# Kernel tuning notes

Hardware: AMD Instinct MI355X
Metric: run time of the kernel (lower is better)

## Reference

```python
import jax, jax.numpy as jnp
import numpy as np

D_MODEL = 1024
N_HEAD = 16
HEAD_SIZE = D_MODEL // N_HEAD
BLOCK_SIZE = 1024
NORM_EPS = 1e-6
B, T = 4, 1024


def setup_inputs() -> dict:
    key = jax.random.key(0)
    ks = jax.random.split(key, 16)
    s = 0.02
    d, h = D_MODEL, 4 * D_MODEL
    return {
        "x":  jax.random.normal(ks[0], (B, T, d), jnp.float32),
        "Wq": jax.random.normal(ks[1], (d, d), jnp.float32) * s,
        "bq": jax.random.normal(ks[2], (d,), jnp.float32) * s,
        "Wk": jax.random.normal(ks[3], (d, d), jnp.float32) * s,
        "bk": jax.random.normal(ks[4], (d,), jnp.float32) * s,
        "Wv": jax.random.normal(ks[5], (d, d), jnp.float32) * s,
        "bv": jax.random.normal(ks[6], (d,), jnp.float32) * s,
        "Wp": jax.random.normal(ks[7], (d, d), jnp.float32) * s,
        "bp": jax.random.normal(ks[8], (d,), jnp.float32) * s,
        "gamma": jnp.ones((d,), jnp.float32),
        "W1": jax.random.normal(ks[9], (d, h), jnp.float32) * s,
        "b1": jax.random.normal(ks[10], (h,), jnp.float32) * s,
        "W2": jax.random.normal(ks[11], (h, d), jnp.float32) * s,
        "b2": jax.random.normal(ks[12], (d,), jnp.float32) * s,
    }


def _rmsnorm(x, gamma):
    ms = jnp.mean(jnp.square(x), axis=-1, keepdims=True)
    return x * jax.lax.rsqrt(ms + NORM_EPS) * gamma


def _attn(x, Wq, bq, Wk, bk, Wv, bv, Wp, bp, causal):
    b, t, c = x.shape
    q = (x @ Wq + bq).reshape(b, t, N_HEAD, HEAD_SIZE)
    k = (x @ Wk + bk).reshape(b, t, N_HEAD, HEAD_SIZE)
    v = (x @ Wv + bv).reshape(b, t, N_HEAD, HEAD_SIZE)
    # NOTE: source divides by head_size**(-0.5) -> multiply by sqrt(head_size)
    scores = jnp.einsum("bqhd,bkhd->bhqk", q, k) * (HEAD_SIZE ** 0.5)
    if causal:
        tril = jnp.tril(jnp.ones((t, t), bool))
        scores = jnp.where(tril, scores, -jnp.inf)
    att = jax.nn.softmax(scores, axis=-1)
    out = jnp.einsum("bhqk,bkhd->bqhd", att, v).reshape(b, t, c)
    return out @ Wp + bp


def _ffwd(x, W1, b1, W2, b2):
    return jax.nn.leaky_relu(x @ W1 + b1, negative_slope=0.1) @ W2 + b2


def reference(x, Wq, bq, Wk, bk, Wv, bv, Wp, bp, gamma, W1, b1, W2, b2):
    # x_out = x + self_att(norm(x), mask=False)
    a = x + _attn(_rmsnorm(x, gamma), Wq, bq, Wk, bk, Wv, bv, Wp, bp, False)
    # x_out = x + ffwd(norm(x_out))   <- residual from ORIGINAL x (faithful)
    b = x + _ffwd(_rmsnorm(a, gamma), W1, b1, W2, b2)
    # x = x_out + self_att(norm(x_out), mask=True)
    c = b + _attn(_rmsnorm(b, gamma), Wq, bq, Wk, bk, Wv, bv, Wp, bp, True)
    return c
```

## Files before the change

kernel.cpp:

```cpp
#include <hip/hip_runtime.h>
#include <cstdint>
#include <cstddef>

typedef __bf16 bf16_t;
typedef __attribute__((ext_vector_type(8))) __bf16 bf16x8;
typedef __attribute__((ext_vector_type(4))) __bf16 bf16x4;
typedef __attribute__((ext_vector_type(4))) float f32x4;

constexpr int D  = 1024;
constexpr int TT = 1024;
constexpr int BB = 4;
constexpr int NH = 16;
constexpr int HS = 64;
constexpr int MR = BB * TT;
constexpr int HF = 4096;

__device__ inline void gload_lds16(const bf16_t* g, bf16_t* l)
{
    __builtin_amdgcn_global_load_lds(
        (const __attribute__((address_space(1))) void*)g,
        (__attribute__((address_space(3))) void*)l, 16, 0, 0);
}

template<bool LO>
__global__ __launch_bounds__(256) void rmsnorm_kernel(const float* __restrict__ x,
                                                      const float* __restrict__ gamma,
                                                      bf16_t* __restrict__ oh,
                                                      bf16_t* __restrict__ ol)
{
    int row = blockIdx.x;
    int t   = threadIdx.x;
    const float* xr = x + (size_t)row * D;
    float4 xv = *(const float4*)(xr + t * 4);
    float ss = xv.x * xv.x + xv.y * xv.y + xv.z * xv.z + xv.w * xv.w;
#pragma unroll
    for (int m = 1; m < 64; m <<= 1) ss += __shfl_xor(ss, m, 64);
    __shared__ float part[4];
    if ((t & 63) == 0) part[t >> 6] = ss;
    __syncthreads();
    float tot   = part[0] + part[1] + part[2] + part[3];
    float scale = rsqrtf(tot * (1.0f / D) + 1e-6f);
    float4 gv = *(const float4*)(gamma + t * 4);
    float vals[4] = {xv.x * scale * gv.x, xv.y * scale * gv.y,
                     xv.z * scale * gv.z, xv.w * scale * gv.w};
    bf16x4 vh, vl;
#pragma unroll
    for (int j = 0; j < 4; ++j) {
        bf16_t h = (bf16_t)vals[j];
        vh[j] = h;
        vl[j] = (bf16_t)(vals[j] - (float)h);
    }
    *(bf16x4*)(oh + (size_t)row * D + t * 4) = vh;
    if (LO) *(bf16x4*)(ol + (size_t)row * D + t * 4) = vl;
}

__global__ __launch_bounds__(256) void concat_bias_kernel(const float* __restrict__ a,
                                                          const float* __restrict__ b,
                                                          float* __restrict__ o)
{
    int i = blockIdx.x * 256 + threadIdx.x;
    o[i] = i < 1024 ? a[i] : b[i - 1024];
}

template<bool LO>
__global__ __launch_bounds__(256) void convw_kernel(const float* __restrict__ W,
                                                    bf16_t* __restrict__ dH,
                                                    bf16_t* __restrict__ dL,
                                                    int K, int N)
{
    __shared__ float sld[64][65];
    int t = threadIdx.x;
    int k0 = blockIdx.x * 64, n0 = blockIdx.y * 64;
    int kr = t >> 4, nc = (t & 15) * 4;
#pragma unroll
    for (int p = 0; p < 4; ++p) {
        int k = p * 16 + kr;
        float4 v = *(const float4*)(W + (size_t)(k0 + k) * N + n0 + nc);
        sld[k][nc] = v.x; sld[k][nc + 1] = v.y; sld[k][nc + 2] = v.z; sld[k][nc + 3] = v.w;
    }
    __syncthreads();
    int n = t >> 2, kh = (t & 3) * 16;
    bf16x8 h0, l0, h1, l1;
#pragma unroll
    for (int j = 0; j < 8; ++j) {
        float v = sld[kh + j][n];
        bf16_t h = (bf16_t)v;
        h0[j] = h; l0[j] = (bf16_t)(v - (float)h);
    }
#pragma unroll
    for (int j = 0; j < 8; ++j) {
        float v = sld[kh + 8 + j][n];
        bf16_t h = (bf16_t)v;
        h1[j] = h; l1[j] = (bf16_t)(v - (float)h);
    }
    size_t o = (size_t)(n0 + n) * K + k0 + kh;
    *(bf16x8*)(dH + o)     = h0;
    *(bf16x8*)(dH + o + 8) = h1;
    if (LO) {
        *(bf16x8*)(dL + o)     = l0;
        *(bf16x8*)(dL + o + 8) = l1;
    }
}

template<int TN, bool CM, bool ALO, bool WLO, int OUTM, bool RELU, bool RESID>
__global__ __launch_bounds__(256, 2) void gemm_kernel(
    const bf16_t* __restrict__ Ahp, const bf16_t* __restrict__ Alp,
    const bf16_t* __restrict__ Whp, const bf16_t* __restrict__ Wlp,
    const float* __restrict__ bias, const float* resid,
    float* outf, bf16_t* __restrict__ outh, bf16_t* __restrict__ outl,
    int N, int K)
{
    constexpr int NF = TN / 32;
    constexpr int AP = ALO ? 2 : 1;
    constexpr int WP = WLO ? 2 : 1;
    __shared__ bf16_t sA[AP][128][32];
    __shared__ bf16_t sW[WP][TN][32];

    int t = threadIdx.x;
    int l = t & 63, w = t >> 6;
    int lr = l & 15, lg = l >> 4;

    int gx  = gridDim.x;
    int gy  = gridDim.y;
    int nwg = gx * gy;
    int bid = blockIdx.y * gx + blockIdx.x;
    int xcd = bid & 7, idx = bid >> 3;
    int nb, mb;
    if (CM) {
        int cw = gx >> 3;
        mb = idx % gy;
        nb = xcd * cw + idx / gy;
    } else {
        int s = xcd * (nwg >> 3) + idx;
        nb = s % gx; mb = s / gx;
    }
    int m0 = mb * 128, n0 = nb * TN;
    int wr = (w >> 1) * 64, wc = (w & 1) * (TN / 2);

    f32x4 acc[4][NF] = {};

    int srow = (l >> 2);
    int sch  = l & 3;

    for (int kk = 0; kk < K; kk += 32) {
        __syncthreads();
#pragma unroll
        for (int c = 0; c < 2; ++c) {
            int rbase = w * 32 + c * 16;
            int row = rbase + srow;
            int f = (row >> 1) & 3;
            size_t goff = (size_t)row * K + kk + (size_t)((sch ^ f)) * 8;
            gload_lds16(Ahp + (size_t)m0 * K + goff, &sA[0][rbase][0]);
            if (ALO) gload_lds16(Alp + (size_t)m0 * K + goff, &sA[AP - 1][rbase][0]);
        }
#pragma unroll
        for (int c = 0; c < TN / 64; ++c) {
            int rbase = w * (TN / 4) + c * 16;
            int row = rbase + srow;
            int f = (row >> 1) & 3;
            size_t goff = (size_t)row * K + kk + (size_t)((sch ^ f)) * 8;
            gload_lds16(Whp + (size_t)n0 * K + goff, &sW[0][rbase][0]);
            if (WLO) gload_lds16(Wlp + (size_t)n0 * K + goff, &sW[WP - 1][rbase][0]);
        }
        __syncthreads();

        bf16x8 a0[4], a1[4], b0[NF], b1[NF];
#pragma unroll
        for (int m = 0; m < 4; ++m) {
            int row = wr + m * 16 + lr;
            int sl = lg ^ ((row >> 1) & 3);
            a0[m] = *(const bf16x8*)&sA[0][row][sl * 8];
            if (ALO) a1[m] = *(const bf16x8*)&sA[AP - 1][row][sl * 8];
        }
#pragma unroll
        for (int n = 0; n < NF; ++n) {
            int row = wc + n * 16 + lr;
            int sl = lg ^ ((row >> 1) & 3);
            b0[n] = *(const bf16x8*)&sW[0][row][sl * 8];
            if (WLO) b1[n] = *(const bf16x8*)&sW[WP - 1][row][sl * 8];
        }
#pragma unroll
        for (int m = 0; m < 4; ++m)
#pragma unroll
            for (int n = 0; n < NF; ++n)
                acc[m][n] = __builtin_amdgcn_mfma_f32_16x16x32_bf16(a0[m], b0[n], acc[m][n], 0, 0, 0);
        if (WLO) {
#pragma unroll
            for (int m = 0; m < 4; ++m)
#pragma unroll
                for (int n = 0; n < NF; ++n)
                    acc[m][n] = __builtin_amdgcn_mfma_f32_16x16x32_bf16(a0[m], b1[n], acc[m][n], 0, 0, 0);
        }
        if (ALO) {
#pragma unroll
            for (int m = 0; m < 4; ++m)
#pragma unroll
                for (int n = 0; n < NF; ++n)
                    acc[m][n] = __builtin_amdgcn_mfma_f32_16x16x32_bf16(a1[m], b0[n], acc[m][n], 0, 0, 0);
        }
    }

#pragma unroll
    for (int m = 0; m < 4; ++m) {
#pragma unroll
        for (int n = 0; n < NF; ++n) {
            int col = n0 + wc + n * 16 + lr;
            float bv = bias[col];
#pragma unroll
            for (int r = 0; r < 4; ++r) {
                int row = m0 + wr + m * 16 + lg * 4 + r;
                float v = acc[m][n][r] + bv;
                if (RELU)  v = (v >= 0.0f) ? v : 0.1f * v;
                if (RESID) v += resid[(size_t)row * N + col];
                if (OUTM == 0) {
                    outf[(size_t)row * N + col] = v;
                } else if (OUTM == 2) {
                    outh[(size_t)row * N + col] = (bf16_t)v;
                } else {
                    bf16_t h = (bf16_t)v;
                    outh[(size_t)row * N + col] = h;
                    outl[(size_t)row * N + col] = (bf16_t)(v - (float)h);
                }
            }
        }
    }
}

template<bool CAUSAL>
__global__ __launch_bounds__(256, 2) void attn_kernel(
    const bf16_t* __restrict__ qkH, const bf16_t* __restrict__ qkL,
    const bf16_t* __restrict__ vP, bf16_t* __restrict__ oh)
{
    __shared__ bf16_t Vth[2][64][70];
    __shared__ bf16_t Ph[4][32][70];

    int tid = threadIdx.x;
    int b = blockIdx.z;
    int qb, h;
    if (CAUSAL) {
        int y = blockIdx.y;
        qb = (blockIdx.z & 2) ? (7 - (y & 7)) : (y & 7);
        h  = (blockIdx.x << 1) | (y >> 3);
    } else {
        h  = blockIdx.x;
        qb = blockIdx.y;
    }
    int l = tid & 63, w = tid >> 6;
    int lr = l & 15, lg = l >> 4;
    int qbase = qb * 128;
    const int QKS = 2 * D;

    bf16x8 aqh[2][2], aql[2][2];
#pragma unroll
    for (int m = 0; m < 2; ++m) {
        size_t qoff = (size_t)(b * TT + qbase + w * 32 + m * 16 + lr) * QKS + h * HS;
#pragma unroll
        for (int c = 0; c < 2; ++c) {
            aqh[m][c] = *(const bf16x8*)(qkH + qoff + c * 32 + lg * 8);
            aql[m][c] = *(const bf16x8*)(qkL + qoff + c * 32 + lg * 8);
        }
    }

    float mrow[2][4], lsum[2][4];
    f32x4 acc_o[2][4] = {};
#pragma unroll
    for (int m = 0; m < 2; ++m)
#pragma unroll
        for (int r = 0; r < 4; ++r) { mrow[m][r] = -1e30f; lsum[m][r] = 0.0f; }

    int ktmax = CAUSAL ? (2 * qb + 1) : (TT / 64 - 1);

    int vrow = tid >> 3;
    int vcol = (tid & 7) * 8;

    bf16x8 vreg[2];
#pragma unroll
    for (int rr = 0; rr < 2; ++rr)
        vreg[rr] = *(const bf16x8*)(vP + (size_t)(b * TT + vrow + rr * 32) * D + h * HS + vcol);
#pragma unroll
    for (int rr = 0; rr < 2; ++rr)
#pragma unroll
        for (int j = 0; j < 8; ++j) Vth[0][vcol + j][vrow + rr * 32] = vreg[rr][j];

    bf16x8 kh0[4], kl0[4], kh1[4], kl1[4];
    {
        size_t koff = (size_t)(b * TT + lr) * QKS + D + h * HS;
#pragma unroll
        for (int nt = 0; nt < 4; ++nt) {
            size_t ko = koff + (size_t)(nt * 16) * QKS;
            kh0[nt] = *(const bf16x8*)(qkH + ko + lg * 8);
            kl0[nt] = *(const bf16x8*)(qkL + ko + lg * 8);
            kh1[nt] = *(const bf16x8*)(qkH + ko + 32 + lg * 8);
            kl1[nt] = *(const bf16x8*)(qkL + ko + 32 + lg * 8);
        }
    }
    __syncthreads();
    int cur = 0;

    for (int kt = 0; kt <= ktmax; ++kt) {
        int kbase = kt * 64;
        int ktn = kt < ktmax ? kt + 1 : ktmax;

#pragma unroll
        for (int rr = 0; rr < 2; ++rr)
            vreg[rr] = *(const bf16x8*)(vP + (size_t)(b * TT + ktn * 64 + vrow + rr * 32) * D + h * HS + vcol);

        f32x4 accs[2][4];
#pragma unroll
        for (int nt = 0; nt < 4; ++nt) {
            __builtin_amdgcn_s_setprio(1);
#pragma unroll
            for (int m = 0; m < 2; ++m) {
                f32x4 s = {};
                s = __builtin_amdgcn_mfma_f32_16x16x32_bf16(aqh[m][0], kh0[nt], s, 0, 0, 0);
                s = __builtin_amdgcn_mfma_f32_16x16x32_bf16(aqh[m][0], kl0[nt], s, 0, 0, 0);
                s = __builtin_amdgcn_mfma_f32_16x16x32_bf16(aql[m][0], kh0[nt], s, 0, 0, 0);
                s = __builtin_amdgcn_mfma_f32_16x16x32_bf16(aqh[m][1], kh1[nt], s, 0, 0, 0);
                s = __builtin_amdgcn_mfma_f32_16x16x32_bf16(aqh[m][1], kl1[nt], s, 0, 0, 0);
                s = __builtin_amdgcn_mfma_f32_16x16x32_bf16(aql[m][1], kh1[nt], s, 0, 0, 0);
                accs[m][nt] = s * 8.0f;
            }
            __builtin_amdgcn_s_setprio(0);
        }

        {
            size_t koffn = (size_t)(b * TT + ktn * 64 + lr) * QKS + D + h * HS;
#pragma unroll
            for (int nt = 0; nt < 4; ++nt) {
                size_t ko = koffn + (size_t)(nt * 16) * QKS;
                kh0[nt] = *(const bf16x8*)(qkH + ko + lg * 8);
                kl0[nt] = *(const bf16x8*)(qkL + ko + lg * 8);
                kh1[nt] = *(const bf16x8*)(qkH + ko + 32 + lg * 8);
                kl1[nt] = *(const bf16x8*)(qkL + ko + 32 + lg * 8);
            }
        }

        if (CAUSAL && kt >= 2 * qb) {
#pragma unroll
            for (int m = 0; m < 2; ++m)
#pragma unroll
                for (int nt = 0; nt < 4; ++nt)
#pragma unroll
                    for (int r = 0; r < 4; ++r) {
                        int qrow = qbase + w * 32 + m * 16 + lg * 4 + r;
                        int kcol = kbase + nt * 16 + lr;
                        if (kcol > qrow) accs[m][nt][r] = -1e30f;
                    }
        }

#pragma unroll
        for (int m = 0; m < 2; ++m) {
            float alpha[4];
#pragma unroll
            for (int r = 0; r < 4; ++r) {
                float mx = fmaxf(fmaxf(accs[m][0][r], accs[m][1][r]),
                                 fmaxf(accs[m][2][r], accs[m][3][r]));
#pragma unroll
                for (int msk = 1; msk < 16; msk <<= 1) mx = fmaxf(mx, __shfl_xor(mx, msk, 64));
                float mnew = fmaxf(mrow[m][r], mx);
                float sum = 0.0f;
#pragma unroll
                for (int nt = 0; nt < 4; ++nt) {
                    float p = __expf(accs[m][nt][r] - mnew);
                    accs[m][nt][r] = p;
                    sum += p;
                }
#pragma unroll
                for (int msk = 1; msk < 16; msk <<= 1) sum += __shfl_xor(sum, msk, 64);
                alpha[r] = __expf(mrow[m][r] - mnew);
                lsum[m][r] = lsum[m][r] * alpha[r] + sum;
                mrow[m][r] = mnew;
            }
#pragma unroll
            for (int et = 0; et < 4; ++et)
#pragma unroll
                for (int r = 0; r < 4; ++r) acc_o[m][et][r] *= alpha[r];

#pragma unroll
            for (int nt = 0; nt < 4; ++nt)
#pragma unroll
                for (int r = 0; r < 4; ++r)
                    Ph[w][m * 16 + lg * 4 + r][nt * 16 + lr] = (bf16_t)accs[m][nt][r];
        }

#pragma unroll
        for (int m = 0; m < 2; ++m) {
            bf16x8 ap0 = *(const bf16x8*)&Ph[w][m * 16 + lr][lg * 8];
            bf16x8 ap1 = *(const bf16x8*)&Ph[w][m * 16 + lr][32 + lg * 8];
            __builtin_amdgcn_s_setprio(1);
#pragma unroll
            for (int et = 0; et < 4; ++et) {
                bf16x8 bv0 = *(const bf16x8*)&Vth[cur][et * 16 + lr][lg * 8];
                bf16x8 bv1 = *(const bf16x8*)&Vth[cur][et * 16 + lr][32 + lg * 8];
                acc_o[m][et] = __builtin_amdgcn_mfma_f32_16x16x32_bf16(ap0, bv0, acc_o[m][et], 0, 0, 0);
                acc_o[m][et] = __builtin_amdgcn_mfma_f32_16x16x32_bf16(ap1, bv1, acc_o[m][et], 0, 0, 0);
            }
            __builtin_amdgcn_s_setprio(0);
        }

#pragma unroll
        for (int rr = 0; rr < 2; ++rr)
#pragma unroll
            for (int j = 0; j < 8; ++j) Vth[cur ^ 1][vcol + j][vrow + rr * 32] = vreg[rr][j];
        __syncthreads();
        cur ^= 1;
    }

#pragma unroll
    for (int m = 0; m < 2; ++m) {
        size_t obase = (size_t)(b * TT + qbase + w * 32 + m * 16) * D + h * HS;
#pragma unroll
        for (int r = 0; r < 4; ++r) {
            float inv = 1.0f / lsum[m][r];
#pragma unroll
            for (int et = 0; et < 4; ++et) {
                float v = acc_o[m][et][r] * inv;
                size_t idx = obase + (size_t)(lg * 4 + r) * D + et * 16 + lr;
                oh[idx] = (bf16_t)v;
            }
        }
    }
}

extern "C" void kernel_launch(void* const* d_in, const int* in_sizes, int n_in,
                              void* d_out, int out_size, void* d_ws, size_t ws_size,
                              hipStream_t stream)
{
    const float* x     = (const float*)d_in[0];
    const float* Wq    = (const float*)d_in[1];
    const float* bq    = (const float*)d_in[2];
    const float* Wk    = (const float*)d_in[3];
    const float* bk    = (const float*)d_in[4];
    const float* Wv    = (const float*)d_in[5];
    const float* bv    = (const float*)d_in[6];
    const float* Wp    = (const float*)d_in[7];
    const float* bp    = (const float*)d_in[8];
    const float* gamma = (const float*)d_in[9];
    const float* W1    = (const float*)d_in[10];
    const float* b1    = (const float*)d_in[11];
    const float* W2    = (const float*)d_in[12];
    const float* b2    = (const float*)d_in[13];
    float* out = (float*)d_out;

    char* base = (char*)d_ws;
    bf16_t* nrmH  = (bf16_t*)(base);
    bf16_t* nrmL  = (bf16_t*)(base + (8u  << 20));
    bf16_t* qkH   = (bf16_t*)(base + (16u << 20));
    bf16_t* qkL   = (bf16_t*)(base + (32u << 20));
    bf16_t* vH    = (bf16_t*)(base + (48u << 20));
    bf16_t* h1H   = (bf16_t*)(base + (16u << 20));
    bf16_t* w1sl  = (bf16_t*)(base + (48u << 20));
    float*  bias2 = (float*)(base + (64u << 20));
    bf16_t* w2sl  = (bf16_t*)(base + (64u << 20));
    bf16_t* wsl   = (bf16_t*)(base + (80u << 20));
    bf16_t* aoH = nrmH;
    float* abuf = out;
    float* bbuf = out;

    size_t DD = (size_t)D * D;
    bf16_t* wqkH = wsl;
    bf16_t* wqkL = wsl + 2 * DD;
    bf16_t* wvH  = wsl + 4 * DD;
    bf16_t* wpH  = wsl + 5 * DD;

    dim3 blk(256);
    dim3 gcvD(D / 64, D / 64);
    dim3 gcv1(D / 64, HF / 64);
    dim3 gcv2(HF / 64, D / 64);
    dim3 gQK(2 * D / 128, MR / 128);
    dim3 gP(D / 64, MR / 128);
    dim3 gF(HF / 128, MR / 128);
    dim3 gAnc(NH, TT / 128, BB);
    dim3 gAc(TT / 128, NH, BB);

    rmsnorm_kernel<true><<<MR, blk, 0, stream>>>(x, gamma, nrmH, nrmL);
    concat_bias_kernel<<<8, blk, 0, stream>>>(bq, bk, bias2);
    convw_kernel<true><<<gcvD, blk, 0, stream>>>(Wq, wqkH,      wqkL,      D, D);
    convw_kernel<true><<<gcvD, blk, 0, stream>>>(Wk, wqkH + DD, wqkL + DD, D, D);
    convw_kernel<false><<<gcvD, blk, 0, stream>>>(Wv, wvH, nullptr, D, D);
    convw_kernel<false><<<gcvD, blk, 0, stream>>>(Wp, wpH, nullptr, D, D);
    gemm_kernel<128, false, true, true, 1, false, false><<<gQK, blk, 0, stream>>>(nrmH, nrmL, wqkH, wqkL, bias2, nullptr, nullptr, qkH, qkL, 2 * D, D);
    gemm_kernel<64, false, false, false, 2, false, false><<<gP, blk, 0, stream>>>(nrmH, nullptr, wvH, nullptr, bv, nullptr, nullptr, vH, nullptr, D, D);
    attn_kernel<false><<<gAnc, blk, 0, stream>>>(qkH, qkL, vH, aoH);
    gemm_kernel<64, false, false, false, 0, false, true><<<gP, blk, 0, stream>>>(aoH, nullptr, wpH, nullptr, bp, x, abuf, nullptr, nullptr, D, D);

    rmsnorm_kernel<false><<<MR, blk, 0, stream>>>(abuf, gamma, nrmH, nullptr);
    convw_kernel<false><<<gcv1, blk, 0, stream>>>(W1, w1sl, nullptr, D, HF);
    gemm_kernel<128, true, false, false, 2, true, false><<<gF, blk, 0, stream>>>(nrmH, nullptr, w1sl, nullptr, b1, nullptr, nullptr, h1H, nullptr, HF, D);
    convw_kernel<false><<<gcv2, blk, 0, stream>>>(W2, w2sl, nullptr, HF, D);
    gemm_kernel<64, false, false, false, 0, false, true><<<gP, blk, 0, stream>>>(h1H, nullptr, w2sl, nullptr, b2, x, bbuf, nullptr, nullptr, D, HF);

    rmsnorm_kernel<true><<<MR, blk, 0, stream>>>(bbuf, gamma, nrmH, nrmL);
    concat_bias_kernel<<<8, blk, 0, stream>>>(bq, bk, bias2);
    gemm_kernel<128, false, true, true, 1, false, false><<<gQK, blk, 0, stream>>>(nrmH, nrmL, wqkH, wqkL, bias2, nullptr, nullptr, qkH, qkL, 2 * D, D);
    gemm_kernel<64, false, false, false, 2, false, false><<<gP, blk, 0, stream>>>(nrmH, nullptr, wvH, nullptr, bv, nullptr, nullptr, vH, nullptr, D, D);
    attn_kernel<true><<<gAc, blk, 0, stream>>>(qkH, qkL, vH, aoH);
    gemm_kernel<64, false, false, false, 0, false, true><<<gP, blk, 0, stream>>>(aoH, nullptr, wpH, nullptr, bp, bbuf, out, nullptr, nullptr, D, D);
}
```

Before: 500.5 us.

## Merge weight conversions, prescale Q, use DPP row reductions in attention

```diff
diff --git a/kernel.cpp b/kernel.cpp
--- a/kernel.cpp
+++ b/kernel.cpp
@@ -20,6 +20,14 @@
     __builtin_amdgcn_global_load_lds(
         (const __attribute__((address_space(1))) void*)g,
         (__attribute__((address_space(3))) void*)l, 16, 0, 0);
+}
+
+template<int N>
+__device__ inline float dpp_ror(float x)
+{
+    int v = __builtin_amdgcn_update_dpp(0, __float_as_int(x),
+                                        0x120 | N, 0xf, 0xf, false);
+    return __int_as_float(v);
 }
 
 template<bool LO>
@@ -94,6 +102,53 @@
         h1[j] = h; l1[j] = (bf16_t)(v - (float)h);
     }
     size_t o = (size_t)(n0 + n) * K + k0 + kh;
+    *(bf16x8*)(dH + o)     = h0;
+    *(bf16x8*)(dH + o + 8) = h1;
+    if (LO) {
+        *(bf16x8*)(dL + o)     = l0;
+        *(bf16x8*)(dL + o + 8) = l1;
+    }
+}
+
+__global__ __launch_bounds__(256) void convw4_kernel(
+    const float* __restrict__ Wq, const float* __restrict__ Wk,
+    const float* __restrict__ Wv, const float* __restrict__ Wp,
+    bf16_t* __restrict__ wqkH, bf16_t* __restrict__ wqkL,
+    bf16_t* __restrict__ wvH, bf16_t* __restrict__ wpH)
+{
+    __shared__ float sld[64][65];
+    int z = blockIdx.z;
+    size_t DD = (size_t)D * D;
+    const float* W = (z == 0) ? Wq : (z == 1) ? Wk : (z == 2) ? Wv : Wp;
+    bf16_t* dH = (z == 0) ? wqkH : (z == 1) ? (wqkH + DD) : (z == 2) ? wvH : wpH;
+    bf16_t* dL = (z == 0) ? wqkL : (z == 1) ? (wqkL + DD) : nullptr;
+    bool LO = (z < 2);
+
+    int t = threadIdx.x;
+    int k0 = blockIdx.x * 64, n0 = blockIdx.y * 64;
+    int kr = t >> 4, nc = (t & 15) * 4;
+#pragma unroll
+    for (int p = 0; p < 4; ++p) {
+        int k = p * 16 + kr;
+        float4 v = *(const float4*)(W + (size_t)(k0 + k) * D + n0 + nc);
+        sld[k][nc] = v.x; sld[k][nc + 1] = v.y; sld[k][nc + 2] = v.z; sld[k][nc + 3] = v.w;
+    }
+    __syncthreads();
+    int n = t >> 2, kh = (t & 3) * 16;
+    bf16x8 h0, l0, h1, l1;
+#pragma unroll
+    for (int j = 0; j < 8; ++j) {
+        float v = sld[kh + j][n];
+        bf16_t h = (bf16_t)v;
+        h0[j] = h; l0[j] = (bf16_t)(v - (float)h);
+    }
+#pragma unroll
+    for (int j = 0; j < 8; ++j) {
+        float v = sld[kh + 8 + j][n];
+        bf16_t h = (bf16_t)v;
+        h1[j] = h; l1[j] = (bf16_t)(v - (float)h);
+    }
+    size_t o = (size_t)(n0 + n) * D + k0 + kh;
     *(bf16x8*)(dH + o)     = h0;
     *(bf16x8*)(dH + o + 8) = h1;
     if (LO) {
@@ -256,8 +311,15 @@
         size_t qoff = (size_t)(b * TT + qbase + w * 32 + m * 16 + lr) * QKS + h * HS;
 #pragma unroll
         for (int c = 0; c < 2; ++c) {
-            aqh[m][c] = *(const bf16x8*)(qkH + qoff + c * 32 + lg * 8);
-            aql[m][c] = *(const bf16x8*)(qkL + qoff + c * 32 + lg * 8);
+            bf16x8 qh = *(const bf16x8*)(qkH + qoff + c * 32 + lg * 8);
+            bf16x8 ql = *(const bf16x8*)(qkL + qoff + c * 32 + lg * 8);
+#pragma unroll
+            for (int j = 0; j < 8; ++j) {
+                qh[j] = (bf16_t)((float)qh[j] * 8.0f);
+                ql[j] = (bf16_t)((float)ql[j] * 8.0f);
+            }
+            aqh[m][c] = qh;
+            aql[m][c] = ql;
         }
     }
 
@@ -318,7 +380,7 @@
                 s = __builtin_amdgcn_mfma_f32_16x16x32_bf16(aqh[m][1], kh1[nt], s, 0, 0, 0);
                 s = __builtin_amdgcn_mfma_f32_16x16x32_bf16(aqh[m][1], kl1[nt], s, 0, 0, 0);
                 s = __builtin_amdgcn_mfma_f32_16x16x32_bf16(aql[m][1], kh1[nt], s, 0, 0, 0);
-                accs[m][nt] = s * 8.0f;
+                accs[m][nt] = s;
             }
             __builtin_amdgcn_s_setprio(0);
         }
@@ -355,8 +417,10 @@
             for (int r = 0; r < 4; ++r) {
                 float mx = fmaxf(fmaxf(accs[m][0][r], accs[m][1][r]),
                                  fmaxf(accs[m][2][r], accs[m][3][r]));
-#pragma unroll
-                for (int msk = 1; msk < 16; msk <<= 1) mx = fmaxf(mx, __shfl_xor(mx, msk, 64));
+                mx = fmaxf(mx, dpp_ror<1>(mx));
+                mx = fmaxf(mx, dpp_ror<2>(mx));
+                mx = fmaxf(mx, dpp_ror<4>(mx));
+                mx = fmaxf(mx, dpp_ror<8>(mx));
                 float mnew = fmaxf(mrow[m][r], mx);
                 float sum = 0.0f;
 #pragma unroll
@@ -365,8 +429,10 @@
                     accs[m][nt][r] = p;
                     sum += p;
                 }
-#pragma unroll
-                for (int msk = 1; msk < 16; msk <<= 1) sum += __shfl_xor(sum, msk, 64);
+                sum += dpp_ror<1>(sum);
+                sum += dpp_ror<2>(sum);
+                sum += dpp_ror<4>(sum);
+                sum += dpp_ror<8>(sum);
                 alpha[r] = __expf(mrow[m][r] - mnew);
                 lsum[m][r] = lsum[m][r] * alpha[r] + sum;
                 mrow[m][r] = mnew;
@@ -464,7 +530,7 @@
     bf16_t* wpH  = wsl + 5 * DD;
 
     dim3 blk(256);
-    dim3 gcvD(D / 64, D / 64);
+    dim3 gcv4(D / 64, D / 64, 4);
     dim3 gcv1(D / 64, HF / 64);
     dim3 gcv2(HF / 64, D / 64);
     dim3 gQK(2 * D / 128, MR / 128);
@@ -475,10 +541,7 @@
 
     rmsnorm_kernel<true><<<MR, blk, 0, stream>>>(x, gamma, nrmH, nrmL);
     concat_bias_kernel<<<8, blk, 0, stream>>>(bq, bk, bias2);
-    convw_kernel<true><<<gcvD, blk, 0, stream>>>(Wq, wqkH,      wqkL,      D, D);
-    convw_kernel<true><<<gcvD, blk, 0, stream>>>(Wk, wqkH + DD, wqkL + DD, D, D);
-    convw_kernel<false><<<gcvD, blk, 0, stream>>>(Wv, wvH, nullptr, D, D);
-    convw_kernel<false><<<gcvD, blk, 0, stream>>>(Wp, wpH, nullptr, D, D);
+    convw4_kernel<<<gcv4, blk, 0, stream>>>(Wq, Wk, Wv, Wp, wqkH, wqkL, wvH, wpH);
     gemm_kernel<128, false, true, true, 1, false, false><<<gQK, blk, 0, stream>>>(nrmH, nrmL, wqkH, wqkL, bias2, nullptr, nullptr, qkH, qkL, 2 * D, D);
     gemm_kernel<64, false, false, false, 2, false, false><<<gP, blk, 0, stream>>>(nrmH, nullptr, wvH, nullptr, bv, nullptr, nullptr, vH, nullptr, D, D);
     attn_kernel<false><<<gAnc, blk, 0, stream>>>(qkH, qkL, vH, aoH);
```

After: 480.8 us. 3.9% less time.
